# Kernel tuning notes

Measured on AMD Instinct MI355X. Metric: run time of the kernel, lower is better.

## Reference

```python
import jax, jax.numpy as jnp
import numpy as np

SMOOTH_STEP_PARAM = 1.0  # = 1/gamma in the TEL paper
DEPTH = 6


def smooth_step(x):
    # TEL smooth-step: 0 for u<=-1/2, 1 for u>=1/2, cubic -2u^3+1.5u+0.5 inside.
    u = SMOOTH_STEP_PARAM * x
    inner = (-2.0 * u + 1.5) * u * u + (u + 0.5) * 0.0 + (-2.0 * u ** 3 + 1.5 * u + 0.5)
    # use single clean expression for the cubic
    cubic = -2.0 * u ** 3 + 1.5 * u + 0.5
    return jnp.where(u <= -0.5, 0.0, jnp.where(u >= 0.5, 1.0, cubic))


def setup_inputs() -> dict:
    key = jax.random.key(0)
    k1, k2, k3 = jax.random.split(key, 3)
    B, D, T, O = 32768, 1024, 8, 128
    num_leaves = 2 ** DEPTH
    x = jax.random.normal(k1, (B, D), dtype=jnp.float32)
    # RandomUniform(-0.01, 0.01) initializers in the original layer
    node_weights = jax.random.uniform(k2, (T, D, num_leaves - 1), dtype=jnp.float32,
                                      minval=-0.01, maxval=0.01)
    leaf_weights = jax.random.uniform(k3, (T, O, num_leaves), dtype=jnp.float32,
                                      minval=-0.01, maxval=0.01)
    return {"x": x, "node_weights": node_weights, "leaf_weights": leaf_weights}


def reference(x, node_weights, leaf_weights):
    B = x.shape[0]
    T = node_weights.shape[0]
    # routing probabilities at every internal node (BFS order): [B, T, 2^depth-1]
    s = smooth_step(jnp.einsum('bd,tdi->bti', x, node_weights))
    # accumulate leaf reach probabilities level by level (left child gets s)
    mu = jnp.ones((B, T, 1), dtype=x.dtype)
    start = 0
    for level in range(DEPTH):
        width = 2 ** level
        s_lvl = s[:, :, start:start + width]           # [B, T, width]
        mu = jnp.stack([mu * s_lvl, mu * (1.0 - s_lvl)], axis=-1)
        mu = mu.reshape(B, T, 2 * width)
        start += width
    # weighted sum of leaf vectors, summed over trees (sum_outputs=True)
    return jnp.einsum('btl,tol->bo', mu, leaf_weights)
```

## Files before the change

### kernel.cpp

```cpp
#include <hip/hip_runtime.h>
#include <hip/hip_bf16.h>
#include <stdint.h>

#define KDIM 1024
#define XSTR2 520
#define TSTR 72
#define RSTR 584

typedef __attribute__((ext_vector_type(4))) float f32x4;
typedef __attribute__((ext_vector_type(8))) short bf16x8;

#define WS_LB_OFF ((size_t)1 << 20)

__device__ __forceinline__ unsigned short f2bf_rne(float f) {
    unsigned u = __float_as_uint(f);
    u = (u + 0x7fffu + ((u >> 16) & 1u)) >> 16;
    return (unsigned short)u;
}

__device__ __forceinline__ unsigned int pack2_bf16(float a, float b) {
    __hip_bfloat162 h = __float22bfloat162_rn(make_float2(a, b));
    union { __hip_bfloat162 h; unsigned int u; } cv;
    cv.h = h;
    return cv.u;
}

__device__ __forceinline__ float gs_get(const uint4* q, int i) {
    uint4 v = q[i >> 3];
    int c = (i >> 1) & 3;
    unsigned w = (c == 0) ? v.x : (c == 1) ? v.y : (c == 2) ? v.z : v.w;
    return __uint_as_float((i & 1) ? (w & 0xffff0000u) : (w << 16));
}

__global__ void prep_w(const float* __restrict__ nw, unsigned short* __restrict__ wb) {
    int idx = blockIdx.x * 256 + threadIdx.x;
    int e    = idx & 7;
    int lane = (idx >> 3) & 63;
    int cb   = (idx >> 9) & 31;
    int ks   = idx >> 14;
    int col = cb * 16 + (lane & 15);
    int k   = ks * 32 + (lane >> 4) * 8 + e;
    int t = col >> 6, i = col & 63;
    float v = (i < 63) ? nw[(t * KDIM + k) * 63 + i] : 0.0f;
    wb[idx] = f2bf_rne(v);
}

__global__ void prep_l(const float* __restrict__ lw, unsigned short* __restrict__ lb) {
    int idx = blockIdx.x * 256 + threadIdx.x;
    int e    = idx & 7;
    int lane = (idx >> 3) & 63;
    int obk  = (idx >> 9) & 7;
    int kq   = idx >> 12;
    int o = obk * 16 + (lane & 15);
    int c = kq * 32 + (lane >> 4) * 8 + e;
    int t = c >> 6, l = c & 63;
    lb[idx] = f2bf_rne(lw[(t * 128 + o) * 64 + l]);
}

__launch_bounds__(1024, 4)
__global__ void fused(const float* __restrict__ x, const unsigned short* __restrict__ wb,
                      const unsigned short* __restrict__ lb, float* __restrict__ out) {
    __shared__ union __align__(16) {
        unsigned short xs[64 * XSTR2];
        unsigned short st[32 * RSTR];
    } sm;

    const int tid  = threadIdx.x;
    const int wave = tid >> 6, lane = tid & 63;
    const int quad = lane >> 4, l16 = lane & 15;
    const int mb   = blockIdx.x;

    f32x4 acc[2][4];
    const f32x4 z4 = {0.f, 0.f, 0.f, 0.f};
    #pragma unroll
    for (int a = 0; a < 2; ++a)
        #pragma unroll
        for (int b = 0; b < 4; ++b) acc[a][b] = z4;

    const int srow = tid >> 4, sf4 = tid & 15;
    const float* xgr = x + (size_t)(mb * 64 + srow) * KDIM;
    const unsigned short* wb0 = wb + ((size_t)(wave * 2) * 64 + lane) * 8;

    for (int h = 0; h < 2; ++h) {
        if (h) __syncthreads();
        #pragma unroll
        for (int seg = 0; seg < 8; ++seg) {
            int f4 = sf4 + seg * 16;
            f32x4 v = __builtin_nontemporal_load((const f32x4*)(xgr + h * 512 + f4 * 4));
            uint2 pk;
            pk.x = pack2_bf16(v[0], v[1]);
            pk.y = pack2_bf16(v[2], v[3]);
            *(uint2*)&sm.xs[srow * XSTR2 + f4 * 4] = pk;
        }
        __syncthreads();
        #pragma unroll 4
        for (int ksl = 0; ksl < 16; ++ksl) {
            const int ks = h * 16 + ksl;
            bf16x8 bf[4], af[2];
            #pragma unroll
            for (int rt = 0; rt < 4; ++rt)
                bf[rt] = *(const bf16x8*)&sm.xs[(rt * 16 + l16) * XSTR2 + ksl * 32 + quad * 8];
            const unsigned short* wbase = wb0 + (size_t)ks * 16384;
            af[0] = *(const bf16x8*)(wbase);
            af[1] = *(const bf16x8*)(wbase + 512);
            #pragma unroll
            for (int ct = 0; ct < 2; ++ct)
                #pragma unroll
                for (int rt = 0; rt < 4; ++rt)
                    acc[ct][rt] = __builtin_amdgcn_mfma_f32_16x16x32_bf16(af[ct], bf[rt], acc[ct][rt], 0, 0, 0);
        }
    }

    #pragma unroll
    for (int p = 0; p < 2; ++p) {
        __syncthreads();
        #pragma unroll
        for (int rt2 = 0; rt2 < 2; ++rt2) {
            int r = rt2 * 16 + l16;
            #pragma unroll
            for (int ct = 0; ct < 2; ++ct) {
                int colb = wave * 32 + ct * 16 + quad * 4;
                f32x4 a = acc[ct][p * 2 + rt2];
                float s0[4];
                #pragma unroll
                for (int j = 0; j < 4; ++j) {
                    float u = a[j];
                    u = fminf(fmaxf(u, -0.5f), 0.5f);
                    s0[j] = u * (1.5f - 2.0f * u * u) + 0.5f;
                }
                uint2 pk;
                pk.x = pack2_bf16(s0[0], s0[1]);
                pk.y = pack2_bf16(s0[2], s0[3]);
                *(uint2*)&sm.st[r * RSTR + (colb >> 6) * TSTR + (colb & 63)] = pk;
            }
        }
        __syncthreads();
        if (tid < 256) {
            int r = tid >> 3, t = tid & 7;
            unsigned short* base = &sm.st[r * RSTR + t * TSTR];
            uint4 q[8];
            #pragma unroll
            for (int c = 0; c < 8; ++c) q[c] = *(const uint4*)(base + c * 8);
            float mu[32];
            mu[0] = 1.0f;
            int start = 0;
            #pragma unroll
            for (int lvl = 0; lvl < 5; ++lvl) {
                int width = 1 << lvl;
                #pragma unroll
                for (int j = width - 1; j >= 0; --j) {
                    float m = mu[j], s_ = gs_get(q, start + j);
                    mu[2 * j + 1] = m * (1.0f - s_);
                    mu[2 * j]     = m * s_;
                }
                start += width;
            }
            #pragma unroll
            for (int c = 0; c < 8; ++c) {
                unsigned pk2[4];
                #pragma unroll
                for (int e = 0; e < 4; ++e) {
                    int j = c * 4 + e;
                    float m = mu[j], s_ = gs_get(q, 31 + j);
                    pk2[e] = pack2_bf16(m * s_, m * (1.0f - s_));
                }
                uint4 v; v.x = pk2[0]; v.y = pk2[1]; v.z = pk2[2]; v.w = pk2[3];
                *(uint4*)(base + c * 8) = v;
            }
        }
        __syncthreads();
        {
            int rtile = wave & 1, obk = wave >> 1;
            int mr = rtile * 16 + l16;
            f32x4 a2 = z4;
            #pragma unroll
            for (int kq = 0; kq < 16; ++kq) {
                int c0 = kq * 32 + quad * 8;
                bf16x8 bmu = *(const bf16x8*)&sm.st[mr * RSTR + (c0 >> 6) * TSTR + (c0 & 63)];
                bf16x8 alf = *(const bf16x8*)(lb + ((size_t)((kq * 8 + obk) * 64 + lane)) * 8);
                a2 = __builtin_amdgcn_mfma_f32_16x16x32_bf16(alf, bmu, a2, 0, 0, 0);
            }
            int rowg = mb * 64 + p * 32 + rtile * 16 + l16;
            int og = obk * 16 + quad * 4;
            __builtin_nontemporal_store(a2, (f32x4*)(out + (size_t)rowg * 128 + og));
        }
    }
}

extern "C" void kernel_launch(void* const* d_in, const int* in_sizes, int n_in,
                              void* d_out, int out_size, void* d_ws, size_t ws_size,
                              hipStream_t stream) {
    const float* x  = (const float*)d_in[0];
    const float* nw = (const float*)d_in[1];
    const float* lw = (const float*)d_in[2];
    float* out = (float*)d_out;

    unsigned short* wb = (unsigned short*)d_ws;
    unsigned short* lb = (unsigned short*)((char*)d_ws + WS_LB_OFF);

    prep_w<<<2048, 256, 0, stream>>>(nw, wb);
    prep_l<<<256, 256, 0, stream>>>(lw, lb);
    fused<<<512, 1024, 0, stream>>>(x, wb, lb, out);
}
```

Baseline: 234.6 us.

## Prefetch second x half during first GEMM half, merge prep kernels, single-pass epilogue

Merges the two weight-prep kernels into one launch to save a kernel launch. In the fused kernel, the second half of x is loaded into registers before computing the first half, and written into a second LDS buffer, so global latency overlaps MFMA work. The epilogue now processes all 64 rows in one pass, with 512 threads doing the tree recursion and each wave computing two output blocks, which removes a loop and several barriers. LDS usage grows (two x buffers, a 64-row st buffer), and the added prefetch registers may reduce occupancy.

```diff
diff --git a/kernel.cpp b/kernel.cpp
--- a/kernel.cpp
+++ b/kernel.cpp
@@ -32,37 +32,61 @@
     return __uint_as_float((i & 1) ? (w & 0xffff0000u) : (w << 16));
 }
 
-__global__ void prep_w(const float* __restrict__ nw, unsigned short* __restrict__ wb) {
-    int idx = blockIdx.x * 256 + threadIdx.x;
-    int e    = idx & 7;
-    int lane = (idx >> 3) & 63;
-    int cb   = (idx >> 9) & 31;
-    int ks   = idx >> 14;
-    int col = cb * 16 + (lane & 15);
-    int k   = ks * 32 + (lane >> 4) * 8 + e;
-    int t = col >> 6, i = col & 63;
-    float v = (i < 63) ? nw[(t * KDIM + k) * 63 + i] : 0.0f;
-    wb[idx] = f2bf_rne(v);
-}
-
-__global__ void prep_l(const float* __restrict__ lw, unsigned short* __restrict__ lb) {
-    int idx = blockIdx.x * 256 + threadIdx.x;
-    int e    = idx & 7;
-    int lane = (idx >> 3) & 63;
-    int obk  = (idx >> 9) & 7;
-    int kq   = idx >> 12;
-    int o = obk * 16 + (lane & 15);
-    int c = kq * 32 + (lane >> 4) * 8 + e;
-    int t = c >> 6, l = c & 63;
-    lb[idx] = f2bf_rne(lw[(t * 128 + o) * 64 + l]);
+__global__ void prep(const float* __restrict__ nw, const float* __restrict__ lw,
+                     unsigned short* __restrict__ wb, unsigned short* __restrict__ lb) {
+    int b = blockIdx.x;
+    if (b < 2048) {
+        int idx = b * 256 + threadIdx.x;
+        int e    = idx & 7;
+        int lane = (idx >> 3) & 63;
+        int cb   = (idx >> 9) & 31;
+        int ks   = idx >> 14;
+        int col = cb * 16 + (lane & 15);
+        int k   = ks * 32 + (lane >> 4) * 8 + e;
+        int t = col >> 6, i = col & 63;
+        float v = (i < 63) ? nw[(t * KDIM + k) * 63 + i] : 0.0f;
+        wb[idx] = f2bf_rne(v);
+    } else {
+        int idx = (b - 2048) * 256 + threadIdx.x;
+        int e    = idx & 7;
+        int lane = (idx >> 3) & 63;
+        int obk  = (idx >> 9) & 7;
+        int kq   = idx >> 12;
+        int o = obk * 16 + (lane & 15);
+        int c = kq * 32 + (lane >> 4) * 8 + e;
+        int t = c >> 6, l = c & 63;
+        lb[idx] = f2bf_rne(lw[(t * 128 + o) * 64 + l]);
+    }
+}
+
+__device__ __forceinline__ void compute_half(const unsigned short* __restrict__ xb,
+                                             const unsigned short* __restrict__ wb0,
+                                             int ksbase, int l16, int quad,
+                                             f32x4 (&acc)[2][4]) {
+    #pragma unroll 4
+    for (int ksl = 0; ksl < 16; ++ksl) {
+        const int ks = ksbase + ksl;
+        bf16x8 bf[4], af[2];
+        #pragma unroll
+        for (int rt = 0; rt < 4; ++rt)
+            bf[rt] = *(const bf16x8*)&xb[(rt * 16 + l16) * XSTR2 + ksl * 32 + quad * 8];
+        const unsigned short* wbase = wb0 + (size_t)ks * 16384;
+        af[0] = *(const bf16x8*)(wbase);
+        af[1] = *(const bf16x8*)(wbase + 512);
+        #pragma unroll
+        for (int ct = 0; ct < 2; ++ct)
+            #pragma unroll
+            for (int rt = 0; rt < 4; ++rt)
+                acc[ct][rt] = __builtin_amdgcn_mfma_f32_16x16x32_bf16(af[ct], bf[rt], acc[ct][rt], 0, 0, 0);
+    }
 }
 
 __launch_bounds__(1024, 4)
 __global__ void fused(const float* __restrict__ x, const unsigned short* __restrict__ wb,
                       const unsigned short* __restrict__ lb, float* __restrict__ out) {
     __shared__ union __align__(16) {
-        unsigned short xs[64 * XSTR2];
-        unsigned short st[32 * RSTR];
+        unsigned short xs[2][64 * XSTR2];
+        unsigned short st[64 * RSTR];
     } sm;
 
     const int tid  = threadIdx.x;
@@ -81,108 +105,115 @@
     const float* xgr = x + (size_t)(mb * 64 + srow) * KDIM;
     const unsigned short* wb0 = wb + ((size_t)(wave * 2) * 64 + lane) * 8;
 
-    for (int h = 0; h < 2; ++h) {
-        if (h) __syncthreads();
-        #pragma unroll
-        for (int seg = 0; seg < 8; ++seg) {
-            int f4 = sf4 + seg * 16;
-            f32x4 v = __builtin_nontemporal_load((const f32x4*)(xgr + h * 512 + f4 * 4));
+    #pragma unroll
+    for (int seg = 0; seg < 8; ++seg) {
+        int f4 = sf4 + seg * 16;
+        f32x4 v = __builtin_nontemporal_load((const f32x4*)(xgr + f4 * 4));
+        uint2 pk;
+        pk.x = pack2_bf16(v[0], v[1]);
+        pk.y = pack2_bf16(v[2], v[3]);
+        *(uint2*)&sm.xs[0][srow * XSTR2 + f4 * 4] = pk;
+    }
+    __syncthreads();
+
+    f32x4 pre[8];
+    #pragma unroll
+    for (int seg = 0; seg < 8; ++seg) {
+        int f4 = sf4 + seg * 16;
+        pre[seg] = __builtin_nontemporal_load((const f32x4*)(xgr + 512 + f4 * 4));
+    }
+
+    compute_half(sm.xs[0], wb0, 0, l16, quad, acc);
+
+    #pragma unroll
+    for (int seg = 0; seg < 8; ++seg) {
+        int f4 = sf4 + seg * 16;
+        uint2 pk;
+        pk.x = pack2_bf16(pre[seg][0], pre[seg][1]);
+        pk.y = pack2_bf16(pre[seg][2], pre[seg][3]);
+        *(uint2*)&sm.xs[1][srow * XSTR2 + f4 * 4] = pk;
+    }
+    __syncthreads();
+
+    compute_half(sm.xs[1], wb0, 16, l16, quad, acc);
+
+    __syncthreads();
+    #pragma unroll
+    for (int rt = 0; rt < 4; ++rt) {
+        int r = rt * 16 + l16;
+        #pragma unroll
+        for (int ct = 0; ct < 2; ++ct) {
+            int colb = wave * 32 + ct * 16 + quad * 4;
+            f32x4 a = acc[ct][rt];
+            float s0[4];
+            #pragma unroll
+            for (int j = 0; j < 4; ++j) {
+                float u = a[j];
+                u = fminf(fmaxf(u, -0.5f), 0.5f);
+                s0[j] = u * (1.5f - 2.0f * u * u) + 0.5f;
+            }
             uint2 pk;
-            pk.x = pack2_bf16(v[0], v[1]);
-            pk.y = pack2_bf16(v[2], v[3]);
-            *(uint2*)&sm.xs[srow * XSTR2 + f4 * 4] = pk;
-        }
-        __syncthreads();
-        #pragma unroll 4
-        for (int ksl = 0; ksl < 16; ++ksl) {
-            const int ks = h * 16 + ksl;
-            bf16x8 bf[4], af[2];
-            #pragma unroll
-            for (int rt = 0; rt < 4; ++rt)
-                bf[rt] = *(const bf16x8*)&sm.xs[(rt * 16 + l16) * XSTR2 + ksl * 32 + quad * 8];
-            const unsigned short* wbase = wb0 + (size_t)ks * 16384;
-            af[0] = *(const bf16x8*)(wbase);
-            af[1] = *(const bf16x8*)(wbase + 512);
-            #pragma unroll
-            for (int ct = 0; ct < 2; ++ct)
-                #pragma unroll
-                for (int rt = 0; rt < 4; ++rt)
-                    acc[ct][rt] = __builtin_amdgcn_mfma_f32_16x16x32_bf16(af[ct], bf[rt], acc[ct][rt], 0, 0, 0);
-        }
-    }
-
-    #pragma unroll
-    for (int p = 0; p < 2; ++p) {
-        __syncthreads();
-        #pragma unroll
-        for (int rt2 = 0; rt2 < 2; ++rt2) {
-            int r = rt2 * 16 + l16;
-            #pragma unroll
-            for (int ct = 0; ct < 2; ++ct) {
-                int colb = wave * 32 + ct * 16 + quad * 4;
-                f32x4 a = acc[ct][p * 2 + rt2];
-                float s0[4];
-                #pragma unroll
-                for (int j = 0; j < 4; ++j) {
-                    float u = a[j];
-                    u = fminf(fmaxf(u, -0.5f), 0.5f);
-                    s0[j] = u * (1.5f - 2.0f * u * u) + 0.5f;
-                }
-                uint2 pk;
-                pk.x = pack2_bf16(s0[0], s0[1]);
-                pk.y = pack2_bf16(s0[2], s0[3]);
-                *(uint2*)&sm.st[r * RSTR + (colb >> 6) * TSTR + (colb & 63)] = pk;
-            }
-        }
-        __syncthreads();
-        if (tid < 256) {
-            int r = tid >> 3, t = tid & 7;
-            unsigned short* base = &sm.st[r * RSTR + t * TSTR];
-            uint4 q[8];
-            #pragma unroll
-            for (int c = 0; c < 8; ++c) q[c] = *(const uint4*)(base + c * 8);
-            float mu[32];
-            mu[0] = 1.0f;
-            int start = 0;
-            #pragma unroll
-            for (int lvl = 0; lvl < 5; ++lvl) {
-                int width = 1 << lvl;
-                #pragma unroll
-                for (int j = width - 1; j >= 0; --j) {
-                    float m = mu[j], s_ = gs_get(q, start + j);
-                    mu[2 * j + 1] = m * (1.0f - s_);
-                    mu[2 * j]     = m * s_;
-                }
-                start += width;
-            }
-            #pragma unroll
-            for (int c = 0; c < 8; ++c) {
-                unsigned pk2[4];
-                #pragma unroll
-                for (int e = 0; e < 4; ++e) {
-                    int j = c * 4 + e;
-                    float m = mu[j], s_ = gs_get(q, 31 + j);
-                    pk2[e] = pack2_bf16(m * s_, m * (1.0f - s_));
-                }
-                uint4 v; v.x = pk2[0]; v.y = pk2[1]; v.z = pk2[2]; v.w = pk2[3];
-                *(uint4*)(base + c * 8) = v;
-            }
-        }
-        __syncthreads();
-        {
-            int rtile = wave & 1, obk = wave >> 1;
-            int mr = rtile * 16 + l16;
-            f32x4 a2 = z4;
-            #pragma unroll
-            for (int kq = 0; kq < 16; ++kq) {
-                int c0 = kq * 32 + quad * 8;
-                bf16x8 bmu = *(const bf16x8*)&sm.st[mr * RSTR + (c0 >> 6) * TSTR + (c0 & 63)];
+            pk.x = pack2_bf16(s0[0], s0[1]);
+            pk.y = pack2_bf16(s0[2], s0[3]);
+            *(uint2*)&sm.st[r * RSTR + (colb >> 6) * TSTR + (colb & 63)] = pk;
+        }
+    }
+    __syncthreads();
+    if (tid < 512) {
+        int r = tid >> 3, t = tid & 7;
+        unsigned short* base = &sm.st[r * RSTR + t * TSTR];
+        uint4 q[8];
+        #pragma unroll
+        for (int c = 0; c < 8; ++c) q[c] = *(const uint4*)(base + c * 8);
+        float mu[32];
+        mu[0] = 1.0f;
+        int start = 0;
+        #pragma unroll
+        for (int lvl = 0; lvl < 5; ++lvl) {
+            int width = 1 << lvl;
+            #pragma unroll
+            for (int j = width - 1; j >= 0; --j) {
+                float m = mu[j], s_ = gs_get(q, start + j);
+                mu[2 * j + 1] = m * (1.0f - s_);
+                mu[2 * j]     = m * s_;
+            }
+            start += width;
+        }
+        #pragma unroll
+        for (int c = 0; c < 8; ++c) {
+            unsigned pk2[4];
+            #pragma unroll
+            for (int e = 0; e < 4; ++e) {
+                int j = c * 4 + e;
+                float m = mu[j], s_ = gs_get(q, 31 + j);
+                pk2[e] = pack2_bf16(m * s_, m * (1.0f - s_));
+            }
+            uint4 v; v.x = pk2[0]; v.y = pk2[1]; v.z = pk2[2]; v.w = pk2[3];
+            *(uint4*)(base + c * 8) = v;
+        }
+    }
+    __syncthreads();
+    {
+        int rtile = wave & 3, obk2 = wave >> 2;
+        int mr = rtile * 16 + l16;
+        f32x4 a2[2];
+        a2[0] = z4; a2[1] = z4;
+        #pragma unroll
+        for (int kq = 0; kq < 16; ++kq) {
+            int c0 = kq * 32 + quad * 8;
+            bf16x8 bmu = *(const bf16x8*)&sm.st[mr * RSTR + (c0 >> 6) * TSTR + (c0 & 63)];
+            #pragma unroll
+            for (int i = 0; i < 2; ++i) {
+                int obk = obk2 * 2 + i;
                 bf16x8 alf = *(const bf16x8*)(lb + ((size_t)((kq * 8 + obk) * 64 + lane)) * 8);
-                a2 = __builtin_amdgcn_mfma_f32_16x16x32_bf16(alf, bmu, a2, 0, 0, 0);
-            }
-            int rowg = mb * 64 + p * 32 + rtile * 16 + l16;
-            int og = obk * 16 + quad * 4;
-            __builtin_nontemporal_store(a2, (f32x4*)(out + (size_t)rowg * 128 + og));
+                a2[i] = __builtin_amdgcn_mfma_f32_16x16x32_bf16(alf, bmu, a2[i], 0, 0, 0);
+            }
+        }
+        int rowg = mb * 64 + rtile * 16 + l16;
+        #pragma unroll
+        for (int i = 0; i < 2; ++i) {
+            int og = (obk2 * 2 + i) * 16 + quad * 4;
+            __builtin_nontemporal_store(a2[i], (f32x4*)(out + (size_t)rowg * 128 + og));
         }
     }
 }
@@ -198,7 +229,6 @@
     unsigned short* wb = (unsigned short*)d_ws;
     unsigned short* lb = (unsigned short*)((char*)d_ws + WS_LB_OFF);
 
-    prep_w<<<2048, 256, 0, stream>>>(nw, wb);
-    prep_l<<<256, 256, 0, stream>>>(lw, lb);
+    prep<<<2304, 256, 0, stream>>>(nw, lw, wb, lb);
     fused<<<512, 1024, 0, stream>>>(x, wb, lb, out);
 }
```

After: 231.3 us. About the same (-1.4%).
